# Optimization experiments

Measured on AMD Instinct MI355X. Metric: run time of the kernel, lower is better.

The kernel has to match this reference:

```python
import jax, jax.numpy as jnp
import numpy as np

HID, EMB, VOCAB, NLAYERS = 512, 256, 64, 2
BS, SLEN, LLEN = 64, 128, 1024


def _p(key, shape, scale):
    return jax.random.normal(key, shape, dtype=jnp.float32) * scale


def setup_inputs() -> dict:
    key = jax.random.key(0)
    ks = jax.random.split(key, 24)
    s_h = 1.0 / np.sqrt(HID)
    inp = {
        "y": jax.random.randint(ks[0], (BS, SLEN), 0, VOCAB, dtype=jnp.int64),
        "encoder_h": jax.random.normal(ks[1], (BS, LLEN, HID), dtype=jnp.float32),
        # embedding table
        "emb": _p(ks[2], (VOCAB, EMB), 1.0),
        # attention LSTMCell: input = hidden + embedding
        "att_Wih": _p(ks[3], (4 * HID, HID + EMB), s_h),
        "att_Whh": _p(ks[4], (4 * HID, HID), s_h),
        "att_bih": _p(ks[5], (4 * HID,), s_h),
        "att_bhh": _p(ks[6], (4 * HID,), s_h),
        # stacked LSTMCells (NLAYERS, ...)
        "rnn_Wih": _p(ks[7], (NLAYERS, 4 * HID, HID), s_h),
        "rnn_Whh": _p(ks[8], (NLAYERS, 4 * HID, HID), s_h),
        "rnn_bih": _p(ks[9], (NLAYERS, 4 * HID), s_h),
        "rnn_bhh": _p(ks[10], (NLAYERS, 4 * HID), s_h),
        # AttentionContext mlp_s / mlp_h
        "Ws_w": _p(ks[11], (HID, HID), s_h),
        "Ws_b": _p(ks[12], (HID,), s_h),
        "Wh_w": _p(ks[13], (HID, HID), s_h),
        "Wh_b": _p(ks[14], (HID,), s_h),
        # output MLP: Linear(2H -> H), ReLU, Linear(H -> V)
        "W1": _p(ks[15], (HID, 2 * HID), 1.0 / np.sqrt(2 * HID)),
        "b1": _p(ks[16], (HID,), s_h),
        "W2": _p(ks[17], (VOCAB, HID), s_h),
        "b2": _p(ks[18], (VOCAB,), s_h),
    }
    return inp


def _lstm_cell(x, h, c, Wih, Whh, bih, bhh):
    gates = x @ Wih.T + bih + h @ Whh.T + bhh  # (B, 4H)
    i, f, g, o = jnp.split(gates, 4, axis=-1)
    c2 = jax.nn.sigmoid(f) * c + jax.nn.sigmoid(i) * jnp.tanh(g)
    h2 = jax.nn.sigmoid(o) * jnp.tanh(c2)
    return h2, c2


def reference(y, encoder_h, emb, att_Wih, att_Whh, att_bih, att_bhh,
              rnn_Wih, rnn_Whh, rnn_bih, rnn_bhh,
              Ws_w, Ws_b, Wh_w, Wh_b, W1, b1, W2, b2):
    B, S = y.shape
    H = att_Whh.shape[1]
    nl = rnn_Wih.shape[0]
    y_emb = emb[y]  # (B, S, E)
    # mlp_h(encoder_h) is loop-invariant; hoist it (same math as per-step recompute)
    h_e = encoder_h @ Wh_w.T + Wh_b  # (B, L, H)

    def step(carry, x_t):
        h0, c0, hs, cs, att = carry
        rnn_in = jnp.concatenate([x_t, att], axis=-1)  # (B, E+H)
        h0, c0 = _lstm_cell(rnn_in, h0, c0, att_Wih, att_Whh, att_bih, att_bhh)
        prev = h0
        new_h, new_c = [], []
        for l in range(nl):
            hl, cl = _lstm_cell(prev, hs[l], cs[l], rnn_Wih[l], rnn_Whh[l],
                                rnn_bih[l], rnn_bhh[l])
            new_h.append(hl)
            new_c.append(cl)
            prev = hl
        hs2 = jnp.stack(new_h)
        cs2 = jnp.stack(new_c)
        # attention on h_t[-1]
        s_e = prev @ Ws_w.T + Ws_b  # (B, H)
        e = jnp.einsum('bh,blh->bl', s_e, h_e)
        a = jax.nn.softmax(e, axis=-1)
        ctx = jnp.einsum('bl,blh->bh', a, h_e)  # (B, H)
        mlp_in = jnp.concatenate([prev, ctx], axis=-1)  # (B, 2H)
        logits = jax.nn.relu(mlp_in @ W1.T + b1) @ W2.T + b2  # (B, V)
        return (h0, c0, hs2, cs2, ctx), logits

    z = jnp.zeros((B, H), dtype=encoder_h.dtype)
    zz = jnp.zeros((nl, B, H), dtype=encoder_h.dtype)
    init = (z, z, zz, zz, z)
    _, y_out = jax.lax.scan(step, init, jnp.swapaxes(y_emb, 0, 1))  # (S, B, V)
    y_out = jnp.swapaxes(y_out, 0, 1)  # (B, S, V)
    return y_out.reshape(B * S, -1)
```

## Files before the change

kernel.cpp:

```cpp
#include <hip/hip_runtime.h>
#include <hip/hip_fp16.h>

#define HID   512
#define EMB   256
#define VOCAB 64
#define BS    64
#define SLEN  128
#define LLEN  1024
#define G4    2048
#define NB    256
#define NT    512
#define ASTR  66
#define ASZ   (128 * ASTR)

typedef unsigned u32x4 __attribute__((ext_vector_type(4)));

__device__ __forceinline__ u32x4 vldq(const unsigned* p) {
    return *reinterpret_cast<const volatile u32x4*>(p);
}
__device__ __forceinline__ float vld1(const float* p) {
    return *reinterpret_cast<const volatile float*>(p);
}
__device__ __forceinline__ void vst1(float* p, float v) {
    *reinterpret_cast<volatile float*>(p) = v;
}
__device__ __forceinline__ void vstu(unsigned* p, unsigned v) {
    *reinterpret_cast<volatile unsigned*>(p) = v;
}
__device__ __forceinline__ unsigned packh2(float x, float y) {
    __half2 h = __floats2half2_rn(x, y);
    return *reinterpret_cast<unsigned*>(&h);
}

struct SCell { float As[2 * ASZ]; float red[8][10][66]; };
struct SAttn { float u_s[512]; float w_s[32]; float msh[4];
               float accs[16][34]; unsigned enc[32 * 261]; };
struct SLog  { float red[16 * 33]; };
union SMem { SCell c; SAttn a; SLog lg; };

__device__ __forceinline__ void gridbar(unsigned* bar, unsigned nb)
{
    __syncthreads();
    const int t = threadIdx.x;
    if (t < 64) {
        if (t == 0)
            __hip_atomic_store(bar + blockIdx.x, nb, __ATOMIC_RELAXED,
                               __HIP_MEMORY_SCOPE_AGENT);
        for (;;) {
            bool ok = true;
#pragma unroll
            for (int i = 0; i < 4; ++i) {
                unsigned v = __hip_atomic_load(bar + i * 64 + t, __ATOMIC_RELAXED,
                                               __HIP_MEMORY_SCOPE_AGENT);
                ok &= (v >= nb);
            }
            if (__all((int)ok)) break;
            __builtin_amdgcn_s_sleep(1);
        }
    }
    __syncthreads();
}

__global__ __launch_bounds__(256)
void k_embed16T(const int* __restrict__ y, const float* __restrict__ emb,
                __half* __restrict__ xemb16)
{
    int i = blockIdx.x * 256 + threadIdx.x;
    int b  = i & 63;
    int e  = (i >> 6) & 255;
    int ts = i >> 14;
    xemb16[i] = __float2half(emb[y[b * SLEN + ts] * EMB + e]);
}

__global__ __launch_bounds__(256)
void k_cast(const float* __restrict__ src, __half* __restrict__ dst, int n4)
{
    int i = blockIdx.x * 256 + threadIdx.x;
    int stride = gridDim.x * 256;
    for (; i < n4; i += stride) {
        float4 v = reinterpret_cast<const float4*>(src)[i];
        reinterpret_cast<__half2*>(dst)[2 * i]     = __floats2half2_rn(v.x, v.y);
        reinterpret_cast<__half2*>(dst)[2 * i + 1] = __floats2half2_rn(v.z, v.w);
    }
}

__global__ __launch_bounds__(256)
void k_pmat(const float* __restrict__ Whw, const float* __restrict__ Wsw,
            const float* __restrict__ Wsb, float* __restrict__ P,
            float* __restrict__ p0)
{
    const int i = blockIdx.x;
    const int t = threadIdx.x;
    float a0 = 0.f, a1 = 0.f, ap = 0.f;
    for (int h = 0; h < HID; ++h) {
        float whi = Whw[h * HID + i];
        a0 += whi * Wsw[h * HID + t];
        a1 += whi * Wsw[h * HID + t + 256];
        ap += whi * Wsb[h];
    }
    P[i * HID + t]       = a0;
    P[i * HID + t + 256] = a1;
    if (t == 0) p0[i] = ap;
}

__global__ __launch_bounds__(256)
void k_fold(const float* __restrict__ aWih, const float* __restrict__ W1,
            const float* __restrict__ Whw, const float* __restrict__ Whb,
            const float* __restrict__ abih, const float* __restrict__ b1,
            float* __restrict__ Wp, float* __restrict__ W1bp,
            float* __restrict__ bihEff, float* __restrict__ b1eff)
{
    const int r = blockIdx.x;
    const int t = threadIdx.x;
    __shared__ float ssrc[512];
    const float* src;
    float* dst;
    if (r < G4) { src = aWih + (size_t)r * (EMB + HID) + EMB; dst = Wp + (size_t)r * HID; }
    else        { src = W1 + (size_t)(r - G4) * (2 * HID) + HID; dst = W1bp + (size_t)(r - G4) * HID; }
    ssrc[t]       = src[t];
    ssrc[t + 256] = src[t + 256];
    __syncthreads();
    float a0 = 0.f, a1 = 0.f;
    for (int h = 0; h < HID; ++h) {
        const float s = ssrc[h];
        a0 += s * Whw[h * HID + t];
        a1 += s * Whw[h * HID + t + 256];
    }
    dst[t]       = a0;
    dst[t + 256] = a1;
    if (t == 0) {
        float bb = 0.f;
        for (int h = 0; h < HID; ++h) bb += ssrc[h] * Whb[h];
        if (r < G4) bihEff[r] = abih[r] + bb;
        else        b1eff[r - G4] = b1[r - G4] + bb;
    }
}

template<int NTILES, int NR, bool VOL>
__device__ __forceinline__ void segScanT(float* As, const __half* A,
    const float* const* w, float* acc, int wv, int lane)
{
    const int t = threadIdx.x;
    const unsigned* ga = reinterpret_cast<const unsigned*>(A) + (size_t)t * 8;
    const int kRow = t >> 2;
    const int c0   = (t & 3) * 16;
    u32x4 Ra[2], Rb[2];

#define LOADT(R, j) do { const unsigned* _p = ga + (size_t)(j) * 4096;            \
        if (VOL) { R[0] = vldq(_p); R[1] = vldq(_p + 4); }                        \
        else { R[0] = *reinterpret_cast<const u32x4*>(_p);                        \
               R[1] = *reinterpret_cast<const u32x4*>(_p + 4); } } while (0)

    LOADT(Ra, 0);
    __syncthreads();
#pragma unroll
    for (int j = 0; j < NTILES; ++j) {
        float2* dst = reinterpret_cast<float2*>(As + (j & 1) * ASZ + kRow * ASTR + c0);
        const u32x4* R = (j & 1) ? Rb : Ra;
#pragma unroll
        for (int q = 0; q < 2; ++q)
#pragma unroll
            for (int h = 0; h < 4; ++h) {
                unsigned uw = R[q][h];
                dst[q * 4 + h] = __half22float2(*reinterpret_cast<const __half2*>(&uw));
            }
        if (j + 1 < NTILES) { if (j & 1) { LOADT(Ra, j + 1); } else { LOADT(Rb, j + 1); } }
        __syncthreads();
        const float* as = As + (j & 1) * ASZ + (wv * 16) * ASTR + lane;
#pragma unroll
        for (int kk = 0; kk < 16; ++kk) {
            const float a = as[kk * ASTR];
            const int k = j * 128 + wv * 16 + kk;
#pragma unroll
            for (int r = 0; r < NR; ++r)
                acc[r] += a * w[r][k];
        }
    }
#undef LOADT
}

__device__ __forceinline__ void packRows(__half* dstH, int i0, const float (&htmp)[2][64])
{
    const int t = threadIdx.x;
    if (t < 64) {
        const int hl = t >> 5;
        const int b2 = (t & 31) * 2;
        vstu(reinterpret_cast<unsigned*>(dstH) + (size_t)(i0 + hl) * 32 + (t & 31),
             packh2(htmp[hl][b2], htmp[hl][b2 + 1]));
    }
}

__device__ __forceinline__ void phaseA(SMem& sm, int i0,
    const __half* xT, const __half* chatT, const __half* h0rT,
    const float* __restrict__ aWih, const float* __restrict__ Wp,
    const float* __restrict__ aWhh, const float* __restrict__ W1bp,
    const float* __restrict__ bihEff, const float* __restrict__ abhh,
    float* cp, const float* hpartPriv, __half* h0wT, float* hid,
    float (&htmp)[2][64], int wv, int lane)
{
    float acc[10] = {};
    {
        const float* w8[8];
#pragma unroll
        for (int r = 0; r < 8; ++r)
            w8[r] = aWih + (size_t)((r >> 1) * HID + i0 + (r & 1)) * (EMB + HID);
        segScanT<2, 8, false>(sm.c.As, xT, w8, acc, wv, lane);
    }
    {
        const float* w10[10];
#pragma unroll
        for (int r = 0; r < 8; ++r)
            w10[r] = Wp + (size_t)((r >> 1) * HID + i0 + (r & 1)) * HID;
        w10[8] = W1bp + (size_t)i0 * HID;
        w10[9] = W1bp + (size_t)(i0 + 1) * HID;
        segScanT<4, 10, true>(sm.c.As, chatT, w10, acc, wv, lane);
    }
    {
        const float* w8[8];
#pragma unroll
        for (int r = 0; r < 8; ++r)
            w8[r] = aWhh + (size_t)((r >> 1) * HID + i0 + (r & 1)) * HID;
        segScanT<4, 8, true>(sm.c.As, h0rT, w8, acc, wv, lane);
    }
#pragma unroll
    for (int r = 0; r < 10; ++r) sm.c.red[wv][r][lane] = acc[r];
    __syncthreads();
    const int t = threadIdx.x;
    if (t < 128) {
        const int b = t & 63, hl = t >> 6;
        float gs[4];
#pragma unroll
        for (int g = 0; g < 4; ++g) {
            const int row = g * HID + i0 + hl;
            float s = bihEff[row] + abhh[row];
#pragma unroll
            for (int w = 0; w < 8; ++w) s += sm.c.red[w][g * 2 + hl][b];
            gs[g] = s;
        }
        const float ig = 1.f / (1.f + __expf(-gs[0]));
        const float fg = 1.f / (1.f + __expf(-gs[1]));
        const float gg = tanhf(gs[2]);
        const float og = 1.f / (1.f + __expf(-gs[3]));
        const float c2 = fg * cp[hl * 64 + b] + ig * gg;
        cp[hl * 64 + b] = c2;
        htmp[hl][b] = og * tanhf(c2);
    } else if (t < 256) {
        const int b = t & 63, hl = (t >> 6) - 2;
        float s = hpartPriv[hl * 64 + b];
#pragma unroll
        for (int w = 0; w < 8; ++w) s += sm.c.red[w][8 + hl][b];
        vst1(hid + (size_t)b * HID + i0 + hl, fmaxf(s, 0.f));
    }
    __syncthreads();
    packRows(h0wT, i0, htmp);
}

__device__ __forceinline__ void phaseR(SMem& sm, int i0,
    const __half* inT, const __half* recT,
    const float* __restrict__ Wih, const float* __restrict__ Whh,
    const float* __restrict__ bih, const float* __restrict__ bhh,
    float* cp, __half* hOutT, float (&htmp)[2][64], int wv, int lane)
{
    float acc[8] = {};
    {
        const float* w8[8];
#pragma unroll
        for (int r = 0; r < 8; ++r)
            w8[r] = Wih + (size_t)((r >> 1) * HID + i0 + (r & 1)) * HID;
        segScanT<4, 8, true>(sm.c.As, inT, w8, acc, wv, lane);
    }
    {
        const float* w8[8];
#pragma unroll
        for (int r = 0; r < 8; ++r)
            w8[r] = Whh + (size_t)((r >> 1) * HID + i0 + (r & 1)) * HID;
        segScanT<4, 8, true>(sm.c.As, recT, w8, acc, wv, lane);
    }
#pragma unroll
    for (int r = 0; r < 8; ++r) sm.c.red[wv][r][lane] = acc[r];
    __syncthreads();
    const int t = threadIdx.x;
    if (t < 128) {
        const int b = t & 63, hl = t >> 6;
        float gs[4];
#pragma unroll
        for (int g = 0; g < 4; ++g) {
            const int row = g * HID + i0 + hl;
            float s = bih[row] + bhh[row];
#pragma unroll
            for (int w = 0; w < 8; ++w) s += sm.c.red[w][g * 2 + hl][b];
            gs[g] = s;
        }
        const float ig = 1.f / (1.f + __expf(-gs[0]));
        const float fg = 1.f / (1.f + __expf(-gs[1]));
        const float gg = tanhf(gs[2]);
        const float og = 1.f / (1.f + __expf(-gs[3]));
        const float c2 = fg * cp[hl * 64 + b] + ig * gg;
        cp[hl * 64 + b] = c2;
        htmp[hl][b] = og * tanhf(c2);
    }
    __syncthreads();
    packRows(hOutT, i0, htmp);
}

__device__ __forceinline__ void logitsPhase(SMem& sm, int bid,
    const float* hid, const float* __restrict__ W2,
    const float* __restrict__ b2, float* __restrict__ out, int tstep)
{
    const int t  = threadIdx.x;
    const int b  = bid & 63;
    const int vg = bid >> 6;
    const int vp = t >> 5;
    const int kk = t & 31;
    float hreg[16];
    const float* hp = hid + (size_t)b * HID + kk * 16;
#pragma unroll
    for (int k = 0; k < 16; ++k) hreg[k] = vld1(hp + k);
    const float* w = W2 + (size_t)(vg * 16 + vp) * HID + kk * 16;
    float s = 0.f;
#pragma unroll
    for (int k = 0; k < 16; ++k) s += hreg[k] * w[k];
    __syncthreads();
    sm.lg.red[vp * 33 + kk] = s;
    __syncthreads();
    if (t < 16) {
        float acc = b2[vg * 16 + t];
#pragma unroll
        for (int k = 0; k < 32; ++k) acc += sm.lg.red[t * 33 + k];
        out[((size_t)b * SLEN + tstep) * VOCAB + vg * 16 + t] = acc;
    }
}

__device__ __forceinline__ void phaseD(SMem& sm, int i0,
    const __half* prevT, const float* __restrict__ Pm,
    const float* __restrict__ p0v, const float* __restrict__ W1,
    const float* __restrict__ b1eff, float* u, float* hpartPriv,
    int wv, int lane)
{
    float acc[4] = {};
    const float* w4[4];
    w4[0] = Pm + (size_t)i0 * HID;
    w4[1] = Pm + (size_t)(i0 + 1) * HID;
    w4[2] = W1 + (size_t)i0 * (2 * HID);
    w4[3] = W1 + (size_t)(i0 + 1) * (2 * HID);
    segScanT<4, 4, true>(sm.c.As, prevT, w4, acc, wv, lane);
#pragma unroll
    for (int r = 0; r < 4; ++r) sm.c.red[wv][r][lane] = acc[r];
    __syncthreads();
    const int t = threadIdx.x;
    if (t < 256) {
        const int b = t & 63, r = t >> 6;
        float s = 0.f;
#pragma unroll
        for (int w = 0; w < 8; ++w) s += sm.c.red[w][r][b];
        if (r < 2) vst1(u + (size_t)b * HID + i0 + r, s + p0v[i0 + r]);
        else       hpartPriv[(r - 2) * 64 + b] = s + b1eff[i0 + r - 2];
    }
}

__device__ __forceinline__ void phaseE(SMem& sm, int bid,
    const float* u, const __half* __restrict__ enc16,
    float* pm, float* ps, float* pv)
{
    const int t    = threadIdx.x;
    const int b    = bid >> 2;
    const int ch   = bid & 3;
    const int half = t >> 8;
    const int col  = t & 255;
    const int le   = t & 31;
    const int seg  = t >> 5;
    const int sq   = t & 15;
    const int sl   = (t >> 4) & 31;

    sm.a.u_s[t] = vld1(u + (size_t)b * HID + t);
    if (t == 0) { sm.a.msh[0] = -3.0e38f; sm.a.msh[1] = 0.f; sm.a.msh[2] = 0.f; }
    float vx = 0.f, vy = 0.f;

    const uint4* src = reinterpret_cast<const uint4*>(enc16 + ((size_t)b * LLEN + ch * 256) * HID);
    uint4 R[4];
#pragma unroll
    for (int p = 0; p < 4; ++p) R[p] = src[(size_t)sl * 64 + p * 16 + sq];
    __syncthreads();

    for (int blk = 0; blk < 8; ++blk) {
        {
            unsigned* dst = &sm.a.enc[sl * 261];
#pragma unroll
            for (int p = 0; p < 4; ++p) {
                const int c4 = (p * 16 + sq) * 4;
                dst[c4] = R[p].x; dst[c4+1] = R[p].y; dst[c4+2] = R[p].z; dst[c4+3] = R[p].w;
            }
        }
        __syncthreads();
        if (blk < 7) {
#pragma unroll
            for (int p = 0; p < 4; ++p)
                R[p] = src[((size_t)(blk + 1) * 32 + sl) * 64 + p * 16 + sq];
        }
        {
            float eacc = 0.f;
            const unsigned* er = &sm.a.enc[le * 261];
            const float* us = sm.a.u_s;
#pragma unroll
            for (int uu = 0; uu < 16; ++uu) {
                const int uo = seg * 16 + uu;
                unsigned uw = er[uo];
                float2 f2 = __half22float2(*reinterpret_cast<const __half2*>(&uw));
                eacc += us[2 * uo] * f2.x + us[2 * uo + 1] * f2.y;
            }
            sm.a.accs[seg][le] = eacc;
        }
        __syncthreads();
        if (t < 32) {
            float e = 0.f;
#pragma unroll
            for (int s2 = 0; s2 < 16; ++s2) e += sm.a.accs[s2][t];
            float bm = e;
#pragma unroll
            for (int off = 16; off > 0; off >>= 1) bm = fmaxf(bm, __shfl_xor(bm, off));
            const float m_old = sm.a.msh[0];
            const float m_new = fmaxf(m_old, bm);
            const float wl = __expf(e - m_new);
            float sw = wl;
#pragma unroll
            for (int off = 16; off > 0; off >>= 1) sw += __shfl_xor(sw, off);
            sm.a.w_s[t] = wl;
            if (t == 0) {
                const float sc = __expf(m_old - m_new);
                sm.a.msh[2] = sc;
                sm.a.msh[1] = sm.a.msh[1] * sc + sw;
                sm.a.msh[0] = m_new;
            }
        }
        __syncthreads();
        {
            const float sc = sm.a.msh[2];
            vx *= sc; vy *= sc;
#pragma unroll
            for (int ll = 0; ll < 16; ++ll) {
                const int l = half * 16 + ll;
                const float wl = sm.a.w_s[l];
                unsigned uw = sm.a.enc[l * 261 + col];
                float2 f2 = __half22float2(*reinterpret_cast<const __half2*>(&uw));
                vx += wl * f2.x; vy += wl * f2.y;
            }
        }
        __syncthreads();
    }
    if (half == 1) { sm.a.u_s[2 * col] = vx; sm.a.u_s[2 * col + 1] = vy; }
    __syncthreads();
    if (half == 0) {
        vx += sm.a.u_s[2 * col];
        vy += sm.a.u_s[2 * col + 1];
        const int pc = b * 4 + ch;
        vst1(pv + (size_t)pc * HID + 2 * col,     vx);
        vst1(pv + (size_t)pc * HID + 2 * col + 1, vy);
        if (t == 0) { vst1(pm + pc, sm.a.msh[0]); vst1(ps + pc, sm.a.msh[1]); }
    }
}

__device__ __forceinline__ void phaseF(int bid,
    const float* pm, const float* ps, const float* pv, __half* chatT)
{
    const int t = threadIdx.x;
    if (t < 128) {
        const int b = t & 63;
        const int j = bid * 2 + (t >> 6);
        float m[4], sd[4], pvv[4];
#pragma unroll
        for (int c = 0; c < 4; ++c) m[c]   = vld1(pm + b * 4 + c);
#pragma unroll
        for (int c = 0; c < 4; ++c) sd[c]  = vld1(ps + b * 4 + c);
#pragma unroll
        for (int c = 0; c < 4; ++c) pvv[c] = vld1(pv + (size_t)(b * 4 + c) * HID + j);
        float M = fmaxf(fmaxf(m[0], m[1]), fmaxf(m[2], m[3]));
        float den = 0.f, num = 0.f;
#pragma unroll
        for (int c = 0; c < 4; ++c) {
            float e = __expf(m[c] - M);
            den += e * sd[c]; num += e * pvv[c];
        }
        float v = num / den;
        float vn = __shfl_down(v, 1);
        if ((b & 1) == 0)
            vstu(reinterpret_cast<unsigned*>(chatT) + (size_t)j * 32 + (b >> 1),
                 packh2(v, vn));
    }
}

__device__ __forceinline__ void phaseT(SMem& sm, int i0,
    const __half* chatT, const float* __restrict__ W1bp,
    const float* hpartPriv, float* hid, int wv, int lane)
{
    float acc[2] = {};
    const float* w2[2];
    w2[0] = W1bp + (size_t)i0 * HID;
    w2[1] = W1bp + (size_t)(i0 + 1) * HID;
    segScanT<4, 2, true>(sm.c.As, chatT, w2, acc, wv, lane);
    sm.c.red[wv][0][lane] = acc[0];
    sm.c.red[wv][1][lane] = acc[1];
    __syncthreads();
    const int t = threadIdx.x;
    if (t < 128) {
        const int b = t & 63, r = t >> 6;
        float s = hpartPriv[r * 64 + b];
#pragma unroll
        for (int w = 0; w < 8; ++w) s += sm.c.red[w][r][b];
        vst1(hid + (size_t)b * HID + i0 + r, fmaxf(s, 0.f));
    }
}

__global__ __launch_bounds__(NT, 1)
void k_seq(const __half* __restrict__ xemb16, const __half* __restrict__ enc16,
           const float* __restrict__ aWih, const float* __restrict__ aWhh,
           const float* __restrict__ bihEff, const float* __restrict__ abhh,
           const float* __restrict__ rWih, const float* __restrict__ rWhh,
           const float* __restrict__ rbih, const float* __restrict__ rbhh,
           const float* __restrict__ Pm, const float* __restrict__ p0v,
           const float* __restrict__ W1, const float* __restrict__ b1eff,
           const float* __restrict__ Wp, const float* __restrict__ W1bp,
           const float* __restrict__ W2, const float* __restrict__ b2,
           __half* h0T, __half* hs0T, __half* hs1T, __half* chatT,
           float* u, float* hid, float* pv, float* pm, float* ps,
           float* out, unsigned* bar)
{
    __shared__ SMem sm;
    __shared__ float cPriv[3][128];
    __shared__ float hpartPriv[128];
    __shared__ float htmp[2][64];

    const int bid  = blockIdx.x;
    const int i0   = bid * 2;
    const int t0   = threadIdx.x;
    const int wv   = __builtin_amdgcn_readfirstlane(t0 >> 6);
    const int lane = t0 & 63;
    if (t0 < 128) { cPriv[0][t0] = 0.f; cPriv[1][t0] = 0.f; cPriv[2][t0] = 0.f;
                    hpartPriv[t0] = 0.f; }
    __syncthreads();

    unsigned nb = 0;
    for (int t = 0; t < SLEN; ++t) {
        const int par = t & 1;
        const __half* h0r  = h0T  + (size_t)par * 32768;
        __half*       h0w  = h0T  + (size_t)(par ^ 1) * 32768;
        const __half* hs0r = hs0T + (size_t)par * 32768;
        __half*       hs0w = hs0T + (size_t)(par ^ 1) * 32768;
        const __half* hs1r = hs1T + (size_t)par * 32768;
        __half*       hs1w = hs1T + (size_t)(par ^ 1) * 32768;

        phaseA(sm, i0, xemb16 + (size_t)t * BS * EMB, chatT, h0r,
               aWih, Wp, aWhh, W1bp, bihEff, abhh,
               cPriv[0], hpartPriv, h0w, hid, htmp, wv, lane);
        gridbar(bar, ++nb);
        phaseR(sm, i0, h0w, hs0r, rWih, rWhh, rbih, rbhh,
               cPriv[1], hs0w, htmp, wv, lane);
        gridbar(bar, ++nb);
        phaseR(sm, i0, hs0w, hs1r, rWih + (size_t)G4 * HID, rWhh + (size_t)G4 * HID,
               rbih + G4, rbhh + G4, cPriv[2], hs1w, htmp, wv, lane);
        gridbar(bar, ++nb);
        if (t > 0) logitsPhase(sm, bid, hid, W2, b2, out, t - 1);
        phaseD(sm, i0, hs1w, Pm, p0v, W1, b1eff, u, hpartPriv, wv, lane);
        gridbar(bar, ++nb);
        phaseE(sm, bid, u, enc16, pm, ps, pv);
        gridbar(bar, ++nb);
        phaseF(bid, pm, ps, pv, chatT);
        gridbar(bar, ++nb);
    }
    phaseT(sm, i0, chatT, W1bp, hpartPriv, hid, wv, lane);
    gridbar(bar, ++nb);
    logitsPhase(sm, bid, hid, W2, b2, out, SLEN - 1);
}

extern "C" void kernel_launch(void* const* d_in, const int* in_sizes, int n_in,
                              void* d_out, int out_size, void* d_ws, size_t ws_size,
                              hipStream_t stream)
{
    const int*   y    = (const int*)  d_in[0];
    const float* enc  = (const float*)d_in[1];
    const float* emb  = (const float*)d_in[2];
    const float* aWih = (const float*)d_in[3];
    const float* aWhh = (const float*)d_in[4];
    const float* abih = (const float*)d_in[5];
    const float* abhh = (const float*)d_in[6];
    const float* rWih = (const float*)d_in[7];
    const float* rWhh = (const float*)d_in[8];
    const float* rbih = (const float*)d_in[9];
    const float* rbhh = (const float*)d_in[10];
    const float* Wsw  = (const float*)d_in[11];
    const float* Wsb  = (const float*)d_in[12];
    const float* Whw  = (const float*)d_in[13];
    const float* Whb  = (const float*)d_in[14];
    const float* W1   = (const float*)d_in[15];
    const float* b1   = (const float*)d_in[16];
    const float* W2   = (const float*)d_in[17];
    const float* b2   = (const float*)d_in[18];
    float* out = (float*)d_out;

    char* base = (char*)d_ws;
    unsigned* bar = (unsigned*)base;                 base += 4096;
    __half* h0T   = (__half*)base;                   base += 2 * 65536;
    __half* hs0T  = (__half*)base;                   base += 2 * 65536;
    __half* hs1T  = (__half*)base;                   base += 2 * 65536;
    __half* chatT = (__half*)base;                   base += 65536;
    size_t zeroBytes = (size_t)(base - (char*)h0T);
    float* u      = (float*)base;                    base += 131072;
    float* hid    = (float*)base;                    base += 131072;
    float* pv     = (float*)base;                    base += 524288;
    float* pm     = (float*)base;                    base += 1024;
    float* ps     = (float*)base;                    base += 1024;
    float* Pm     = (float*)base;                    base += 1048576;
    float* p0v    = (float*)base;                    base += 2048;
    float* Wp     = (float*)base;                    base += (size_t)G4 * HID * 4;
    float* W1bp   = (float*)base;                    base += (size_t)HID * HID * 4;
    float* bihEff = (float*)base;                    base += 8192;
    float* b1eff  = (float*)base;                    base += 2048;
    __half* xemb16 = (__half*)base;                  base += (size_t)SLEN * BS * EMB * 2;
    __half* enc16  = (__half*)base;                  base += (size_t)BS * LLEN * HID * 2;
    size_t need = (size_t)(base - (char*)d_ws);
    if (ws_size < need) return;

    hipMemsetAsync(bar, 0, 4096, stream);
    hipMemsetAsync(h0T, 0, zeroBytes, stream);

    k_embed16T<<<(SLEN * BS * EMB) / 256, 256, 0, stream>>>(y, emb, xemb16);
    k_cast<<<4096, 256, 0, stream>>>(enc, enc16, (BS * LLEN * HID) / 4);
    k_pmat<<<HID, 256, 0, stream>>>(Whw, Wsw, Wsb, Pm, p0v);
    k_fold<<<G4 + HID, 256, 0, stream>>>(aWih, W1, Whw, Whb, abih, b1,
                                         Wp, W1bp, bihEff, b1eff);

    k_seq<<<NB, NT, 0, stream>>>(xemb16, enc16,
        aWih, aWhh, bihEff, abhh, rWih, rWhh, rbih, rbhh,
        Pm, p0v, W1, b1eff, Wp, W1bp, W2, b2,
        h0T, hs0T, hs1T, chatT, u, hid, pv, pm, ps, out, bar);
}
```

Before: 18.65 ms.

## Split persistent kernel into four independent batch groups with per-group grid barriers

The persistent sequential kernel now runs 512 blocks, split into 4 groups of 128 blocks. Each group owns 16 batch rows, and barrier slots are kept per group, so groups synchronise only among themselves. The batch-major layouts (transposed activations, embeddings, attention partials) are rearranged to match, and each block now handles 4 hidden units for 16 batches. The aim is shorter barriers and more parallelism per step. In exchange, every group streams the full weight matrices separately, which multiplies weight traffic, and occupancy must reach 2+ blocks per CU for all 512 blocks to be co-resident.

```diff
diff --git a/kernel.cpp b/kernel.cpp
--- a/kernel.cpp
+++ b/kernel.cpp
@@ -8,10 +8,14 @@
 #define SLEN  128
 #define LLEN  1024
 #define G4    2048
-#define NB    256
+#define NB    512
 #define NT    512
-#define ASTR  66
-#define ASZ   (128 * ASTR)
+#define NW    8
+#define NG    4
+#define GB    128
+#define BSG   16
+#define ASTR2 18
+#define ASZ2  (256 * ASTR2)
 
 typedef unsigned u32x4 __attribute__((ext_vector_type(4)));
 
@@ -32,25 +36,26 @@
     return *reinterpret_cast<unsigned*>(&h);
 }
 
-struct SCell { float As[2 * ASZ]; float red[8][10][66]; };
+struct SCell { float As[2 * ASZ2]; float red[NW][20][18]; };
 struct SAttn { float u_s[512]; float w_s[32]; float msh[4];
                float accs[16][34]; unsigned enc[32 * 261]; };
-struct SLog  { float red[16 * 33]; };
+struct SLog  { float red[8 * 65]; };
 union SMem { SCell c; SAttn a; SLog lg; };
 
-__device__ __forceinline__ void gridbar(unsigned* bar, unsigned nb)
+__device__ __forceinline__ void gridbar(unsigned* bar, int g, int gbid, unsigned nb)
 {
     __syncthreads();
     const int t = threadIdx.x;
     if (t < 64) {
+        unsigned* slots = bar + g * 256;
         if (t == 0)
-            __hip_atomic_store(bar + blockIdx.x, nb, __ATOMIC_RELAXED,
+            __hip_atomic_store(slots + gbid, nb, __ATOMIC_RELAXED,
                                __HIP_MEMORY_SCOPE_AGENT);
         for (;;) {
             bool ok = true;
 #pragma unroll
-            for (int i = 0; i < 4; ++i) {
-                unsigned v = __hip_atomic_load(bar + i * 64 + t, __ATOMIC_RELAXED,
+            for (int i = 0; i < 2; ++i) {
+                unsigned v = __hip_atomic_load(slots + i * 64 + t, __ATOMIC_RELAXED,
                                                __HIP_MEMORY_SCOPE_AGENT);
                 ok &= (v >= nb);
             }
@@ -66,9 +71,11 @@
                 __half* __restrict__ xemb16)
 {
     int i = blockIdx.x * 256 + threadIdx.x;
-    int b  = i & 63;
-    int e  = (i >> 6) & 255;
-    int ts = i >> 14;
+    int ts  = i >> 14;
+    int g   = (i >> 12) & 3;
+    int e   = (i >> 4) & 255;
+    int b16 = i & 15;
+    int b = g * 16 + b16;
     xemb16[i] = __float2half(emb[y[b * SLEN + ts] * EMB + e]);
 }
 
@@ -138,233 +145,239 @@
 
 template<int NTILES, int NR, bool VOL>
 __device__ __forceinline__ void segScanT(float* As, const __half* A,
-    const float* const* w, float* acc, int wv, int lane)
-{
-    const int t = threadIdx.x;
-    const unsigned* ga = reinterpret_cast<const unsigned*>(A) + (size_t)t * 8;
-    const int kRow = t >> 2;
-    const int c0   = (t & 3) * 16;
-    u32x4 Ra[2], Rb[2];
-
-#define LOADT(R, j) do { const unsigned* _p = ga + (size_t)(j) * 4096;            \
-        if (VOL) { R[0] = vldq(_p); R[1] = vldq(_p + 4); }                        \
-        else { R[0] = *reinterpret_cast<const u32x4*>(_p);                        \
-               R[1] = *reinterpret_cast<const u32x4*>(_p + 4); } } while (0)
-
-    LOADT(Ra, 0);
+    const float* const* w, float* acc, int wv, int lb)
+{
+    const int t = threadIdx.x;
+    const unsigned* ga = reinterpret_cast<const unsigned*>(A)
+                       + (size_t)(t >> 1) * 8 + (t & 1) * 4;
+    const int kRow = t >> 1;
+    const int c0   = (t & 1) * 8;
+    u32x4 Ra, Rb;
+    Ra = VOL ? vldq(ga) : *reinterpret_cast<const u32x4*>(ga);
     __syncthreads();
 #pragma unroll
     for (int j = 0; j < NTILES; ++j) {
-        float2* dst = reinterpret_cast<float2*>(As + (j & 1) * ASZ + kRow * ASTR + c0);
-        const u32x4* R = (j & 1) ? Rb : Ra;
-#pragma unroll
-        for (int q = 0; q < 2; ++q)
+        {
+            float2* dst2 = reinterpret_cast<float2*>(As + (j & 1) * ASZ2 + kRow * ASTR2 + c0);
+            const u32x4 R = (j & 1) ? Rb : Ra;
 #pragma unroll
             for (int h = 0; h < 4; ++h) {
-                unsigned uw = R[q][h];
-                dst[q * 4 + h] = __half22float2(*reinterpret_cast<const __half2*>(&uw));
+                unsigned uw = R[h];
+                dst2[h] = __half22float2(*reinterpret_cast<const __half2*>(&uw));
             }
-        if (j + 1 < NTILES) { if (j & 1) { LOADT(Ra, j + 1); } else { LOADT(Rb, j + 1); } }
+        }
+        if (j + 1 < NTILES) {
+            const unsigned* p = ga + (size_t)(j + 1) * 2048;
+            if (j & 1) Ra = VOL ? vldq(p) : *reinterpret_cast<const u32x4*>(p);
+            else       Rb = VOL ? vldq(p) : *reinterpret_cast<const u32x4*>(p);
+        }
         __syncthreads();
-        const float* as = As + (j & 1) * ASZ + (wv * 16) * ASTR + lane;
-#pragma unroll
-        for (int kk = 0; kk < 16; ++kk) {
-            const float a = as[kk * ASTR];
-            const int k = j * 128 + wv * 16 + kk;
+        const float* as = As + (j & 1) * ASZ2 + (wv * 32) * ASTR2 + lb;
+#pragma unroll
+        for (int kk = 0; kk < 32; ++kk) {
+            const float a = as[kk * ASTR2];
+            const int k = j * 256 + wv * 32 + kk;
 #pragma unroll
             for (int r = 0; r < NR; ++r)
                 acc[r] += a * w[r][k];
         }
     }
-#undef LOADT
-}
-
-__device__ __forceinline__ void packRows(__half* dstH, int i0, const float (&htmp)[2][64])
-{
-    const int t = threadIdx.x;
-    if (t < 64) {
-        const int hl = t >> 5;
-        const int b2 = (t & 31) * 2;
-        vstu(reinterpret_cast<unsigned*>(dstH) + (size_t)(i0 + hl) * 32 + (t & 31),
-             packh2(htmp[hl][b2], htmp[hl][b2 + 1]));
-    }
-}
-
-__device__ __forceinline__ void phaseA(SMem& sm, int i0,
-    const __half* xT, const __half* chatT, const __half* h0rT,
+}
+
+__device__ __forceinline__ void packRows(unsigned* dstU, int g, int i0,
+                                         const float (&htmp)[4][16])
+{
+    const int t = threadIdx.x;
+    if (t < 32) {
+        const int row = t >> 3, pair = t & 7;
+        vstu(dstU + (size_t)g * 4096 + (size_t)(i0 + row) * 8 + pair,
+             packh2(htmp[row][pair * 2], htmp[row][pair * 2 + 1]));
+    }
+}
+
+__device__ __forceinline__ void phaseA(SMem& sm, int g, int i0, int tstep,
+    const __half* xemb16, const __half* chatT, const __half* h0rT,
     const float* __restrict__ aWih, const float* __restrict__ Wp,
     const float* __restrict__ aWhh, const float* __restrict__ W1bp,
     const float* __restrict__ bihEff, const float* __restrict__ abhh,
-    float* cp, const float* hpartPriv, __half* h0wT, float* hid,
-    float (&htmp)[2][64], int wv, int lane)
-{
-    float acc[10] = {};
+    float* cp, const float* hpartPriv, unsigned* h0wU, float* hid,
+    float (&htmp)[4][16], int wv, int lane)
+{
+    const int r  = lane >> 4;
+    const int lb = lane & 15;
+    float acc[5] = {};
     {
-        const float* w8[8];
-#pragma unroll
-        for (int r = 0; r < 8; ++r)
-            w8[r] = aWih + (size_t)((r >> 1) * HID + i0 + (r & 1)) * (EMB + HID);
-        segScanT<2, 8, false>(sm.c.As, xT, w8, acc, wv, lane);
+        const float* w4[4];
+#pragma unroll
+        for (int q = 0; q < 4; ++q)
+            w4[q] = aWih + (size_t)(q * HID + i0 + r) * (EMB + HID);
+        segScanT<1, 4, false>(sm.c.As, xemb16 + (size_t)tstep * 16384 + g * 4096,
+                              w4, acc, wv, lb);
     }
     {
-        const float* w10[10];
-#pragma unroll
-        for (int r = 0; r < 8; ++r)
-            w10[r] = Wp + (size_t)((r >> 1) * HID + i0 + (r & 1)) * HID;
-        w10[8] = W1bp + (size_t)i0 * HID;
-        w10[9] = W1bp + (size_t)(i0 + 1) * HID;
-        segScanT<4, 10, true>(sm.c.As, chatT, w10, acc, wv, lane);
+        const float* w5[5];
+#pragma unroll
+        for (int q = 0; q < 4; ++q)
+            w5[q] = Wp + (size_t)(q * HID + i0 + r) * HID;
+        w5[4] = W1bp + (size_t)(i0 + r) * HID;
+        segScanT<2, 5, true>(sm.c.As, chatT + (size_t)g * 8192, w5, acc, wv, lb);
     }
     {
-        const float* w8[8];
-#pragma unroll
-        for (int r = 0; r < 8; ++r)
-            w8[r] = aWhh + (size_t)((r >> 1) * HID + i0 + (r & 1)) * HID;
-        segScanT<4, 8, true>(sm.c.As, h0rT, w8, acc, wv, lane);
-    }
-#pragma unroll
-    for (int r = 0; r < 10; ++r) sm.c.red[wv][r][lane] = acc[r];
-    __syncthreads();
-    const int t = threadIdx.x;
-    if (t < 128) {
-        const int b = t & 63, hl = t >> 6;
+        const float* w4[4];
+#pragma unroll
+        for (int q = 0; q < 4; ++q)
+            w4[q] = aWhh + (size_t)(q * HID + i0 + r) * HID;
+        segScanT<2, 4, true>(sm.c.As, h0rT + (size_t)g * 8192, w4, acc, wv, lb);
+    }
+#pragma unroll
+    for (int q = 0; q < 4; ++q) sm.c.red[wv][q * 4 + r][lb] = acc[q];
+    sm.c.red[wv][16 + r][lb] = acc[4];
+    __syncthreads();
+    const int t = threadIdx.x;
+    if (t < 64) {
+        const int b = t & 15, rr = t >> 4;
         float gs[4];
 #pragma unroll
-        for (int g = 0; g < 4; ++g) {
-            const int row = g * HID + i0 + hl;
+        for (int q = 0; q < 4; ++q) {
+            const int row = q * HID + i0 + rr;
             float s = bihEff[row] + abhh[row];
 #pragma unroll
-            for (int w = 0; w < 8; ++w) s += sm.c.red[w][g * 2 + hl][b];
-            gs[g] = s;
+            for (int w = 0; w < NW; ++w) s += sm.c.red[w][q * 4 + rr][b];
+            gs[q] = s;
         }
         const float ig = 1.f / (1.f + __expf(-gs[0]));
         const float fg = 1.f / (1.f + __expf(-gs[1]));
         const float gg = tanhf(gs[2]);
         const float og = 1.f / (1.f + __expf(-gs[3]));
-        const float c2 = fg * cp[hl * 64 + b] + ig * gg;
-        cp[hl * 64 + b] = c2;
-        htmp[hl][b] = og * tanhf(c2);
-    } else if (t < 256) {
-        const int b = t & 63, hl = (t >> 6) - 2;
-        float s = hpartPriv[hl * 64 + b];
-#pragma unroll
-        for (int w = 0; w < 8; ++w) s += sm.c.red[w][8 + hl][b];
-        vst1(hid + (size_t)b * HID + i0 + hl, fmaxf(s, 0.f));
-    }
-    __syncthreads();
-    packRows(h0wT, i0, htmp);
-}
-
-__device__ __forceinline__ void phaseR(SMem& sm, int i0,
+        const float c2 = fg * cp[rr * 16 + b] + ig * gg;
+        cp[rr * 16 + b] = c2;
+        htmp[rr][b] = og * tanhf(c2);
+    } else if (t < 128) {
+        const int b = t & 15, rr = (t >> 4) - 4;
+        float s = hpartPriv[rr * 16 + b];
+#pragma unroll
+        for (int w = 0; w < NW; ++w) s += sm.c.red[w][16 + rr][b];
+        vst1(hid + (size_t)(g * 16 + b) * HID + i0 + rr, fmaxf(s, 0.f));
+    }
+    __syncthreads();
+    packRows(h0wU, g, i0, htmp);
+}
+
+__device__ __forceinline__ void phaseR(SMem& sm, int g, int i0,
     const __half* inT, const __half* recT,
     const float* __restrict__ Wih, const float* __restrict__ Whh,
     const float* __restrict__ bih, const float* __restrict__ bhh,
-    float* cp, __half* hOutT, float (&htmp)[2][64], int wv, int lane)
-{
-    float acc[8] = {};
+    float* cp, unsigned* hOutU, float (&htmp)[4][16], int wv, int lane)
+{
+    const int r  = lane >> 4;
+    const int lb = lane & 15;
+    float acc[4] = {};
     {
-        const float* w8[8];
-#pragma unroll
-        for (int r = 0; r < 8; ++r)
-            w8[r] = Wih + (size_t)((r >> 1) * HID + i0 + (r & 1)) * HID;
-        segScanT<4, 8, true>(sm.c.As, inT, w8, acc, wv, lane);
+        const float* w4[4];
+#pragma unroll
+        for (int q = 0; q < 4; ++q)
+            w4[q] = Wih + (size_t)(q * HID + i0 + r) * HID;
+        segScanT<2, 4, true>(sm.c.As, inT + (size_t)g * 8192, w4, acc, wv, lb);
     }
     {
-        const float* w8[8];
-#pragma unroll
-        for (int r = 0; r < 8; ++r)
-            w8[r] = Whh + (size_t)((r >> 1) * HID + i0 + (r & 1)) * HID;
-        segScanT<4, 8, true>(sm.c.As, recT, w8, acc, wv, lane);
-    }
-#pragma unroll
-    for (int r = 0; r < 8; ++r) sm.c.red[wv][r][lane] = acc[r];
-    __syncthreads();
-    const int t = threadIdx.x;
-    if (t < 128) {
-        const int b = t & 63, hl = t >> 6;
+        const float* w4[4];
+#pragma unroll
+        for (int q = 0; q < 4; ++q)
+            w4[q] = Whh + (size_t)(q * HID + i0 + r) * HID;
+        segScanT<2, 4, true>(sm.c.As, recT + (size_t)g * 8192, w4, acc, wv, lb);
+    }
+#pragma unroll
+    for (int q = 0; q < 4; ++q) sm.c.red[wv][q * 4 + r][lb] = acc[q];
+    __syncthreads();
+    const int t = threadIdx.x;
+    if (t < 64) {
+        const int b = t & 15, rr = t >> 4;
         float gs[4];
 #pragma unroll
-        for (int g = 0; g < 4; ++g) {
-            const int row = g * HID + i0 + hl;
+        for (int q = 0; q < 4; ++q) {
+            const int row = q * HID + i0 + rr;
             float s = bih[row] + bhh[row];
 #pragma unroll
-            for (int w = 0; w < 8; ++w) s += sm.c.red[w][g * 2 + hl][b];
-            gs[g] = s;
+            for (int w = 0; w < NW; ++w) s += sm.c.red[w][q * 4 + rr][b];
+            gs[q] = s;
         }
         const float ig = 1.f / (1.f + __expf(-gs[0]));
         const float fg = 1.f / (1.f + __expf(-gs[1]));
         const float gg = tanhf(gs[2]);
         const float og = 1.f / (1.f + __expf(-gs[3]));
-        const float c2 = fg * cp[hl * 64 + b] + ig * gg;
-        cp[hl * 64 + b] = c2;
-        htmp[hl][b] = og * tanhf(c2);
-    }
-    __syncthreads();
-    packRows(hOutT, i0, htmp);
-}
-
-__device__ __forceinline__ void logitsPhase(SMem& sm, int bid,
+        const float c2 = fg * cp[rr * 16 + b] + ig * gg;
+        cp[rr * 16 + b] = c2;
+        htmp[rr][b] = og * tanhf(c2);
+    }
+    __syncthreads();
+    packRows(hOutU, g, i0, htmp);
+}
+
+__device__ __forceinline__ void logitsPhase(SMem& sm, int g, int gbid,
     const float* hid, const float* __restrict__ W2,
     const float* __restrict__ b2, float* __restrict__ out, int tstep)
 {
     const int t  = threadIdx.x;
-    const int b  = bid & 63;
-    const int vg = bid >> 6;
-    const int vp = t >> 5;
-    const int kk = t & 31;
-    float hreg[16];
-    const float* hp = hid + (size_t)b * HID + kk * 16;
-#pragma unroll
-    for (int k = 0; k < 16; ++k) hreg[k] = vld1(hp + k);
-    const float* w = W2 + (size_t)(vg * 16 + vp) * HID + kk * 16;
+    const int b  = gbid & 15;
+    const int vg = gbid >> 4;
+    const int gb = g * 16 + b;
+    const int vp = t >> 6;
+    const int kk = t & 63;
+    float hreg[8];
+    const float* hp = hid + (size_t)gb * HID + kk * 8;
+#pragma unroll
+    for (int k = 0; k < 8; ++k) hreg[k] = vld1(hp + k);
+    const float* w = W2 + (size_t)(vg * 8 + vp) * HID + kk * 8;
     float s = 0.f;
 #pragma unroll
-    for (int k = 0; k < 16; ++k) s += hreg[k] * w[k];
-    __syncthreads();
-    sm.lg.red[vp * 33 + kk] = s;
-    __syncthreads();
-    if (t < 16) {
-        float acc = b2[vg * 16 + t];
-#pragma unroll
-        for (int k = 0; k < 32; ++k) acc += sm.lg.red[t * 33 + k];
-        out[((size_t)b * SLEN + tstep) * VOCAB + vg * 16 + t] = acc;
-    }
-}
-
-__device__ __forceinline__ void phaseD(SMem& sm, int i0,
+    for (int k = 0; k < 8; ++k) s += hreg[k] * w[k];
+    __syncthreads();
+    sm.lg.red[vp * 65 + kk] = s;
+    __syncthreads();
+    if (t < 8) {
+        float acc = b2[vg * 8 + t];
+#pragma unroll
+        for (int k = 0; k < 64; ++k) acc += sm.lg.red[t * 65 + k];
+        out[((size_t)gb * SLEN + tstep) * VOCAB + vg * 8 + t] = acc;
+    }
+    __syncthreads();
+}
+
+__device__ __forceinline__ void phaseD(SMem& sm, int g, int i0,
     const __half* prevT, const float* __restrict__ Pm,
     const float* __restrict__ p0v, const float* __restrict__ W1,
     const float* __restrict__ b1eff, float* u, float* hpartPriv,
     int wv, int lane)
 {
-    float acc[4] = {};
-    const float* w4[4];
-    w4[0] = Pm + (size_t)i0 * HID;
-    w4[1] = Pm + (size_t)(i0 + 1) * HID;
-    w4[2] = W1 + (size_t)i0 * (2 * HID);
-    w4[3] = W1 + (size_t)(i0 + 1) * (2 * HID);
-    segScanT<4, 4, true>(sm.c.As, prevT, w4, acc, wv, lane);
-#pragma unroll
-    for (int r = 0; r < 4; ++r) sm.c.red[wv][r][lane] = acc[r];
-    __syncthreads();
-    const int t = threadIdx.x;
-    if (t < 256) {
-        const int b = t & 63, r = t >> 6;
+    const int r  = lane >> 4;
+    const int lb = lane & 15;
+    float acc[2] = {};
+    const float* w2[2];
+    w2[0] = Pm + (size_t)(i0 + r) * HID;
+    w2[1] = W1 + (size_t)(i0 + r) * (2 * HID);
+    segScanT<2, 2, true>(sm.c.As, prevT + (size_t)g * 8192, w2, acc, wv, lb);
+    sm.c.red[wv][r][lb]     = acc[0];
+    sm.c.red[wv][4 + r][lb] = acc[1];
+    __syncthreads();
+    const int t = threadIdx.x;
+    if (t < 128) {
+        const int b = t & 15, rr = t >> 4;
         float s = 0.f;
 #pragma unroll
-        for (int w = 0; w < 8; ++w) s += sm.c.red[w][r][b];
-        if (r < 2) vst1(u + (size_t)b * HID + i0 + r, s + p0v[i0 + r]);
-        else       hpartPriv[(r - 2) * 64 + b] = s + b1eff[i0 + r - 2];
-    }
-}
-
-__device__ __forceinline__ void phaseE(SMem& sm, int bid,
+        for (int w = 0; w < NW; ++w) s += sm.c.red[w][rr][b];
+        if (rr < 4) vst1(u + (size_t)(g * 16 + b) * HID + i0 + rr, s + p0v[i0 + rr]);
+        else        hpartPriv[(rr - 4) * 16 + b] = s + b1eff[i0 + rr - 4];
+    }
+}
+
+__device__ __forceinline__ void phaseE(SMem& sm, int g, int gbid,
     const float* u, const __half* __restrict__ enc16,
     float* pm, float* ps, float* pv)
 {
     const int t    = threadIdx.x;
-    const int b    = bid >> 2;
-    const int ch   = bid & 3;
+    const int b    = gbid >> 3;
+    const int ch   = gbid & 7;
+    const int gb   = g * 16 + b;
     const int half = t >> 8;
     const int col  = t & 255;
     const int le   = t & 31;
@@ -372,17 +385,17 @@
     const int sq   = t & 15;
     const int sl   = (t >> 4) & 31;
 
-    sm.a.u_s[t] = vld1(u + (size_t)b * HID + t);
+    sm.a.u_s[t] = vld1(u + (size_t)gb * HID + t);
     if (t == 0) { sm.a.msh[0] = -3.0e38f; sm.a.msh[1] = 0.f; sm.a.msh[2] = 0.f; }
     float vx = 0.f, vy = 0.f;
 
-    const uint4* src = reinterpret_cast<const uint4*>(enc16 + ((size_t)b * LLEN + ch * 256) * HID);
+    const uint4* src = reinterpret_cast<const uint4*>(enc16 + ((size_t)gb * LLEN + ch * 128) * HID);
     uint4 R[4];
 #pragma unroll
     for (int p = 0; p < 4; ++p) R[p] = src[(size_t)sl * 64 + p * 16 + sq];
     __syncthreads();
 
-    for (int blk = 0; blk < 8; ++blk) {
+    for (int blk = 0; blk < 4; ++blk) {
         {
             unsigned* dst = &sm.a.enc[sl * 261];
 #pragma unroll
@@ -392,7 +405,7 @@
             }
         }
         __syncthreads();
-        if (blk < 7) {
+        if (blk < 3) {
 #pragma unroll
             for (int p = 0; p < 4; ++p)
                 R[p] = src[((size_t)(blk + 1) * 32 + sl) * 64 + p * 16 + sq];
@@ -452,65 +465,67 @@
     if (half == 0) {
         vx += sm.a.u_s[2 * col];
         vy += sm.a.u_s[2 * col + 1];
-        const int pc = b * 4 + ch;
+        const int pc = gb * 8 + ch;
         vst1(pv + (size_t)pc * HID + 2 * col,     vx);
         vst1(pv + (size_t)pc * HID + 2 * col + 1, vy);
         if (t == 0) { vst1(pm + pc, sm.a.msh[0]); vst1(ps + pc, sm.a.msh[1]); }
     }
 }
 
-__device__ __forceinline__ void phaseF(int bid,
-    const float* pm, const float* ps, const float* pv, __half* chatT)
-{
-    const int t = threadIdx.x;
-    if (t < 128) {
-        const int b = t & 63;
-        const int j = bid * 2 + (t >> 6);
-        float m[4], sd[4], pvv[4];
-#pragma unroll
-        for (int c = 0; c < 4; ++c) m[c]   = vld1(pm + b * 4 + c);
-#pragma unroll
-        for (int c = 0; c < 4; ++c) sd[c]  = vld1(ps + b * 4 + c);
-#pragma unroll
-        for (int c = 0; c < 4; ++c) pvv[c] = vld1(pv + (size_t)(b * 4 + c) * HID + j);
-        float M = fmaxf(fmaxf(m[0], m[1]), fmaxf(m[2], m[3]));
+__device__ __forceinline__ void phaseF(int g, int gbid,
+    const float* pm, const float* ps, const float* pv, unsigned* chatU)
+{
+    const int t = threadIdx.x;
+    if (t < 64) {
+        const int b = t & 15;
+        const int j = gbid * 4 + (t >> 4);
+        const int gb = g * 16 + b;
+        float m[8], sd[8], pvv[8];
+#pragma unroll
+        for (int c = 0; c < 8; ++c) m[c]   = vld1(pm + gb * 8 + c);
+#pragma unroll
+        for (int c = 0; c < 8; ++c) sd[c]  = vld1(ps + gb * 8 + c);
+#pragma unroll
+        for (int c = 0; c < 8; ++c) pvv[c] = vld1(pv + (size_t)(gb * 8 + c) * HID + j);
+        float M = m[0];
+#pragma unroll
+        for (int c = 1; c < 8; ++c) M = fmaxf(M, m[c]);
         float den = 0.f, num = 0.f;
 #pragma unroll
-        for (int c = 0; c < 4; ++c) {
+        for (int c = 0; c < 8; ++c) {
             float e = __expf(m[c] - M);
             den += e * sd[c]; num += e * pvv[c];
         }
         float v = num / den;
         float vn = __shfl_down(v, 1);
-        if ((b & 1) == 0)
-            vstu(reinterpret_cast<unsigned*>(chatT) + (size_t)j * 32 + (b >> 1),
-                 packh2(v, vn));
-    }
-}
-
-__device__ __forceinline__ void phaseT(SMem& sm, int i0,
+        if (!(b & 1))
+            vstu(chatU + (size_t)g * 4096 + (size_t)j * 8 + (b >> 1), packh2(v, vn));
+    }
+}
+
+__device__ __forceinline__ void phaseT(SMem& sm, int g, int i0,
     const __half* chatT, const float* __restrict__ W1bp,
     const float* hpartPriv, float* hid, int wv, int lane)
 {
-    float acc[2] = {};
-    const float* w2[2];
-    w2[0] = W1bp + (size_t)i0 * HID;
-    w2[1] = W1bp + (size_t)(i0 + 1) * HID;
-    segScanT<4, 2, true>(sm.c.As, chatT, w2, acc, wv, lane);
-    sm.c.red[wv][0][lane] = acc[0];
-    sm.c.red[wv][1][lane] = acc[1];
-    __syncthreads();
-    const int t = threadIdx.x;
-    if (t < 128) {
-        const int b = t & 63, r = t >> 6;
-        float s = hpartPriv[r * 64 + b];
-#pragma unroll
-        for (int w = 0; w < 8; ++w) s += sm.c.red[w][r][b];
-        vst1(hid + (size_t)b * HID + i0 + r, fmaxf(s, 0.f));
-    }
-}
-
-__global__ __launch_bounds__(NT, 1)
+    const int r  = lane >> 4;
+    const int lb = lane & 15;
+    float acc[1] = {};
+    const float* w1[1];
+    w1[0] = W1bp + (size_t)(i0 + r) * HID;
+    segScanT<2, 1, true>(sm.c.As, chatT + (size_t)g * 8192, w1, acc, wv, lb);
+    sm.c.red[wv][r][lb] = acc[0];
+    __syncthreads();
+    const int t = threadIdx.x;
+    if (t < 64) {
+        const int b = t & 15, rr = t >> 4;
+        float s = hpartPriv[rr * 16 + b];
+#pragma unroll
+        for (int w = 0; w < NW; ++w) s += sm.c.red[w][rr][b];
+        vst1(hid + (size_t)(g * 16 + b) * HID + i0 + rr, fmaxf(s, 0.f));
+    }
+}
+
+__global__ __launch_bounds__(NT, 4)
 void k_seq(const __half* __restrict__ xemb16, const __half* __restrict__ enc16,
            const float* __restrict__ aWih, const float* __restrict__ aWhh,
            const float* __restrict__ bihEff, const float* __restrict__ abhh,
@@ -525,50 +540,55 @@
            float* out, unsigned* bar)
 {
     __shared__ SMem sm;
-    __shared__ float cPriv[3][128];
-    __shared__ float hpartPriv[128];
-    __shared__ float htmp[2][64];
+    __shared__ float cPriv[3][64];
+    __shared__ float hpartPriv[64];
+    __shared__ float htmp[4][16];
 
     const int bid  = blockIdx.x;
-    const int i0   = bid * 2;
+    const int g    = bid >> 7;
+    const int gbid = bid & 127;
+    const int i0   = gbid * 4;
     const int t0   = threadIdx.x;
     const int wv   = __builtin_amdgcn_readfirstlane(t0 >> 6);
     const int lane = t0 & 63;
-    if (t0 < 128) { cPriv[0][t0] = 0.f; cPriv[1][t0] = 0.f; cPriv[2][t0] = 0.f;
-                    hpartPriv[t0] = 0.f; }
+    if (t0 < 64) { cPriv[0][t0] = 0.f; cPriv[1][t0] = 0.f; cPriv[2][t0] = 0.f;
+                   hpartPriv[t0] = 0.f; }
     __syncthreads();
 
     unsigned nb = 0;
     for (int t = 0; t < SLEN; ++t) {
         const int par = t & 1;
         const __half* h0r  = h0T  + (size_t)par * 32768;
-        __half*       h0w  = h0T  + (size_t)(par ^ 1) * 32768;
+        unsigned*     h0wU = reinterpret_cast<unsigned*>(h0T + (size_t)(par ^ 1) * 32768);
         const __half* hs0r = hs0T + (size_t)par * 32768;
-        __half*       hs0w = hs0T + (size_t)(par ^ 1) * 32768;
+        unsigned*     hs0wU = reinterpret_cast<unsigned*>(hs0T + (size_t)(par ^ 1) * 32768);
+        const __half* hs0w  = hs0T + (size_t)(par ^ 1) * 32768;
         const __half* hs1r = hs1T + (size_t)par * 32768;
-        __half*       hs1w = hs1T + (size_t)(par ^ 1) * 32768;
-
-        phaseA(sm, i0, xemb16 + (size_t)t * BS * EMB, chatT, h0r,
+        unsigned*     hs1wU = reinterpret_cast<unsigned*>(hs1T + (size_t)(par ^ 1) * 32768);
+        const __half* hs1w  = hs1T + (size_t)(par ^ 1) * 32768;
+
+        phaseA(sm, g, i0, t, xemb16, chatT, h0r,
                aWih, Wp, aWhh, W1bp, bihEff, abhh,
-               cPriv[0], hpartPriv, h0w, hid, htmp, wv, lane);
-        gridbar(bar, ++nb);
-        phaseR(sm, i0, h0w, hs0r, rWih, rWhh, rbih, rbhh,
-               cPriv[1], hs0w, htmp, wv, lane);
-        gridbar(bar, ++nb);
-        phaseR(sm, i0, hs0w, hs1r, rWih + (size_t)G4 * HID, rWhh + (size_t)G4 * HID,
-               rbih + G4, rbhh + G4, cPriv[2], hs1w, htmp, wv, lane);
-        gridbar(bar, ++nb);
-        if (t > 0) logitsPhase(sm, bid, hid, W2, b2, out, t - 1);
-        phaseD(sm, i0, hs1w, Pm, p0v, W1, b1eff, u, hpartPriv, wv, lane);
-        gridbar(bar, ++nb);
-        phaseE(sm, bid, u, enc16, pm, ps, pv);
-        gridbar(bar, ++nb);
-        phaseF(bid, pm, ps, pv, chatT);
-        gridbar(bar, ++nb);
-    }
-    phaseT(sm, i0, chatT, W1bp, hpartPriv, hid, wv, lane);
-    gridbar(bar, ++nb);
-    logitsPhase(sm, bid, hid, W2, b2, out, SLEN - 1);
+               cPriv[0], hpartPriv, h0wU, hid, htmp, wv, lane);
+        gridbar(bar, g, gbid, ++nb);
+        phaseR(sm, g, i0, h0T + (size_t)(par ^ 1) * 32768, hs0r,
+               rWih, rWhh, rbih, rbhh, cPriv[1], hs0wU, htmp, wv, lane);
+        gridbar(bar, g, gbid, ++nb);
+        phaseR(sm, g, i0, hs0w, hs1r,
+               rWih + (size_t)G4 * HID, rWhh + (size_t)G4 * HID,
+               rbih + G4, rbhh + G4, cPriv[2], hs1wU, htmp, wv, lane);
+        gridbar(bar, g, gbid, ++nb);
+        if (t > 0) logitsPhase(sm, g, gbid, hid, W2, b2, out, t - 1);
+        phaseD(sm, g, i0, hs1w, Pm, p0v, W1, b1eff, u, hpartPriv, wv, lane);
+        gridbar(bar, g, gbid, ++nb);
+        phaseE(sm, g, gbid, u, enc16, pm, ps, pv);
+        gridbar(bar, g, gbid, ++nb);
+        phaseF(g, gbid, pm, ps, pv, reinterpret_cast<unsigned*>(chatT));
+        gridbar(bar, g, gbid, ++nb);
+    }
+    phaseT(sm, g, i0, chatT, W1bp, hpartPriv, hid, wv, lane);
+    gridbar(bar, g, gbid, ++nb);
+    logitsPhase(sm, g, gbid, hid, W2, b2, out, SLEN - 1);
 }
 
 extern "C" void kernel_launch(void* const* d_in, const int* in_sizes, int n_in,
@@ -605,9 +625,9 @@
     size_t zeroBytes = (size_t)(base - (char*)h0T);
     float* u      = (float*)base;                    base += 131072;
     float* hid    = (float*)base;                    base += 131072;
-    float* pv     = (float*)base;                    base += 524288;
-    float* pm     = (float*)base;                    base += 1024;
-    float* ps     = (float*)base;                    base += 1024;
+    float* pv     = (float*)base;                    base += 1048576;
+    float* pm     = (float*)base;                    base += 2048;
+    float* ps     = (float*)base;                    base += 2048;
     float* Pm     = (float*)base;                    base += 1048576;
     float* p0v    = (float*)base;                    base += 2048;
     float* Wp     = (float*)base;                    base += (size_t)G4 * HID * 4;
```

Result: slower. 42.06 ms (+125.5%).
